# Kernel optimization log

Hardware: AMD Instinct MI355X
Metric: run time of the kernel (lower is better)

## Reference

```python
import jax, jax.numpy as jnp
import numpy as np

B, S, HID = 2, 2048, 1024
H, D = 16, 64
NUM_BUCKETS, MAX_DIST = 32, 128
NEG_INF = -1e9


def _rel_buckets(rel_pos, num_buckets, max_distance):
    # decoder (unidirectional): only non-positive relative positions valid
    rp = -jnp.minimum(rel_pos, 0)  # [q,k] >= 0
    max_exact = num_buckets // 2
    is_small = rp < max_exact
    safe = jnp.maximum(rp, 1).astype(jnp.float32)
    large = max_exact + (
        jnp.log(safe / max_exact) / np.log(max_distance / max_exact) * (num_buckets - max_exact)
    ).astype(jnp.int32)
    large = jnp.minimum(large, num_buckets - 1)
    return jnp.where(is_small, rp, large)


def _rotate_half(t):
    t1, t2 = jnp.split(t, 2, axis=-1)
    return jnp.concatenate([-t2, t1], axis=-1)


def setup_inputs() -> dict:
    key = jax.random.key(0)
    ks = jax.random.split(key, 6)
    sc = 0.02
    x = jax.random.normal(ks[0], (B, S, HID), jnp.float32)
    Wq = jax.random.normal(ks[1], (HID, H * D), jnp.float32) * sc
    Wk = jax.random.normal(ks[2], (HID, H * D), jnp.float32) * sc
    Wv = jax.random.normal(ks[3], (HID, H * D), jnp.float32) * sc
    Wo = jax.random.normal(ks[4], (H * D, HID), jnp.float32) * sc
    rel_bias = jax.random.normal(ks[5], (NUM_BUCKETS, H), jnp.float32) * sc
    # rotary tables: emb = cat(freqs, freqs), non-interleave layout
    inv_freq = 1.0 / (10000.0 ** (np.arange(0, D, 2, dtype=np.float32) / D))
    freqs = np.arange(S, dtype=np.float32)[:, None] * inv_freq[None, :]  # [S, D/2]
    emb = np.concatenate([freqs, freqs], axis=-1)  # [S, D]
    cos = jnp.asarray(np.cos(emb), jnp.float32)
    sin = jnp.asarray(np.sin(emb), jnp.float32)
    return {"x": x, "Wq": Wq, "Wk": Wk, "Wv": Wv, "Wo": Wo,
            "rel_bias": rel_bias, "cos": cos, "sin": sin}


def reference(x, Wq, Wk, Wv, Wo, rel_bias, cos, sin):
    # QKV projections (weights stored [in, out])
    q = (x @ Wq).reshape(B, S, H, D)
    k = (x @ Wk).reshape(B, S, H, D)
    v = (x @ Wv).reshape(B, S, H, D)
    # RoPE (non-interleave): q*cos + rotate_half(q)*sin, cos/sin broadcast over B,H
    c = cos[None, :, None, :]
    s = sin[None, :, None, :]
    q = q * c + _rotate_half(q) * s
    k = k * c + _rotate_half(k) * s
    # scores [B,H,S,S]
    scores = jnp.einsum("bqhd,bkhd->bhqk", q, k) / np.sqrt(D).astype(np.float32)
    # learned relative-position bucket bias (T5-style, decoder/unidirectional)
    ctx_pos = jnp.arange(S)[:, None]
    mem_pos = jnp.arange(S)[None, :]
    buckets = _rel_buckets(mem_pos - ctx_pos, NUM_BUCKETS, MAX_DIST)  # [S,S]
    bias = rel_bias[buckets]  # [S,S,H]
    scores = scores + jnp.transpose(bias, (2, 0, 1))[None]
    # causal mask (decoder self-attention)
    causal = mem_pos <= ctx_pos  # [S,S]
    scores = jnp.where(causal[None, None], scores, NEG_INF)
    attn = jax.nn.softmax(scores, axis=-1)
    ctx = jnp.einsum("bhqk,bkhd->bqhd", attn, v).reshape(B, S, H * D)
    return ctx @ Wo
```

## Files before the change

### kernel.cpp

```cpp
#include <hip/hip_runtime.h>
#include <hip/hip_bf16.h>
#include <math.h>

#define B_   2
#define S_   2048
#define HID_ 1024
#define H_   16
#define D_   64
#define HD_  (H_ * D_)

typedef __attribute__((ext_vector_type(8))) short bf16x8;
typedef __attribute__((ext_vector_type(4))) short bf16x4;
typedef __attribute__((ext_vector_type(4))) float f32x4;
typedef __attribute__((ext_vector_type(4))) unsigned uint4v;
typedef unsigned short u16;

#define LOG2E 1.44269504088896f

static __device__ __forceinline__ u16 f2bf(float f) {
    unsigned u = __builtin_bit_cast(unsigned, f);
    u += 0x7fffu + ((u >> 16) & 1u);
    return (u16)(u >> 16);
}
static __device__ __forceinline__ unsigned cvtpk(float lo, float hi) {
    unsigned r;
    asm("v_cvt_pk_bf16_f32 %0, %1, %2" : "=v"(r) : "v"(lo), "v"(hi));
    return r;
}
static __device__ __forceinline__ int swzK(int row, int colbytes) {
    return row * 128 + (colbytes ^ ((row & 7) << 4));
}
static __device__ __forceinline__ int swzV(int row, int colbytes) {
    return row * 128 + (colbytes ^ ((row & 7) << 4) ^ (((row >> 3) & 1) << 3));
}
static __device__ __forceinline__ void gll16(const void* g, void* l) {
    __builtin_amdgcn_global_load_lds(
        (const __attribute__((address_space(1))) unsigned int*)g,
        (__attribute__((address_space(3))) unsigned int*)l, 16, 0, 0);
}

__global__ __launch_bounds__(256) void prep(const float* __restrict__ x,
                                            u16* __restrict__ xb,
                                            const float* __restrict__ W0,
                                            const float* __restrict__ W1,
                                            const float* __restrict__ W2,
                                            const float* __restrict__ W3,
                                            u16* __restrict__ o0,
                                            u16* __restrict__ o1,
                                            u16* __restrict__ o2,
                                            u16* __restrict__ o3) {
    __shared__ float tS[32][33];
    const int bid = blockIdx.x;
    if (bid < 4096) {
        int i = bid * 256 + threadIdx.x;
        float4 f = ((const float4*)x)[i];
        ushort4 u;
        u.x = f2bf(f.x); u.y = f2bf(f.y); u.z = f2bf(f.z); u.w = f2bf(f.w);
        ((ushort4*)xb)[i] = u;
    } else {
        const int id  = bid - 4096;
        const int z   = id >> 10;
        const int rem = id & 1023;
        const float* in = z == 0 ? W0 : z == 1 ? W1 : z == 2 ? W2 : W3;
        u16* out       = z == 0 ? o0 : z == 1 ? o1 : z == 2 ? o2 : o3;
        const int bx = (rem & 31) * 32, by = (rem >> 5) * 32;
        const int xx = threadIdx.x & 31, yy = threadIdx.x >> 5;
        #pragma unroll
        for (int j = 0; j < 4; j++)
            tS[yy + j * 8][xx] = in[(long)(by + yy + j * 8) * HID_ + bx + xx];
        __syncthreads();
        #pragma unroll
        for (int j = 0; j < 4; j++)
            out[(long)(bx + yy + j * 8) * HID_ + by + xx] = f2bf(tS[xx][yy + j * 8]);
    }
}

__global__ __launch_bounds__(256, 3) void gemm_qkv(const u16* __restrict__ A,
                                                   const u16* __restrict__ Bt,
                                                   u16* __restrict__ outb,
                                                   const float* __restrict__ cosb,
                                                   const float* __restrict__ sinb,
                                                   int K) {
    __shared__ u16 As[128 * 32];
    __shared__ u16 Bs[128 * 32];
    const int t = threadIdx.x;
    const int lane = t & 63;
    const int w = t >> 6;
    const int qlane = lane & 15, grp = lane >> 4;
    const int m0 = blockIdx.y * 128, n0 = blockIdx.x * 128;
    const int wr = w >> 1, wc = w & 1;

    f32x4 acc[4][4];
    #pragma unroll
    for (int i = 0; i < 4; i++)
        #pragma unroll
        for (int j = 0; j < 4; j++) acc[i][j] = (f32x4){0.f, 0.f, 0.f, 0.f};

    const int srow = (lane >> 2);
    const int scol = (lane & 3) * 8;
    const int nkt = K >> 5;
    for (int kt = 0; kt < nkt; kt++) {
        const int k0 = kt << 5;
        #pragma unroll
        for (int c = 0; c < 2; c++) {
            const int chunk = w * 2 + c;
            const int row = chunk * 16 + srow;
            gll16(A  + (long)(m0 + row) * K + k0 + scol, As + chunk * 512);
            gll16(Bt + (long)(n0 + row) * K + k0 + scol, Bs + chunk * 512);
        }
        __syncthreads();
        bf16x8 af[4], bfr[4];
        #pragma unroll
        for (int i = 0; i < 4; i++) {
            af[i]  = *(const bf16x8*)(As + (wr * 64 + i * 16 + qlane) * 32 + grp * 8);
            bfr[i] = *(const bf16x8*)(Bs + (wc * 64 + i * 16 + qlane) * 32 + grp * 8);
        }
        #pragma unroll
        for (int mf = 0; mf < 4; mf++)
            #pragma unroll
            for (int nf = 0; nf < 4; nf++)
                acc[mf][nf] = __builtin_amdgcn_mfma_f32_16x16x32_bf16(bfr[nf], af[mf], acc[mf][nf], 0, 0, 0);
        __syncthreads();
    }

    const int gnb = n0 + wc * 64;
    const bool isqk = gnb < 2048;
    const bool isq  = gnb < 1024;
    const float QS = 0.125f * LOG2E;
    #pragma unroll
    for (int mf = 0; mf < 4; mf++) {
        const int m = m0 + wr * 64 + mf * 16 + qlane;
        if (isqk) {
            const int s = m & (S_ - 1);
            const float* cr = cosb + s * 64;
            const float* sr = sinb + s * 64;
            #pragma unroll
            for (int nf2 = 0; nf2 < 2; nf2++) {
                #pragma unroll
                for (int r = 0; r < 4; r++) {
                    const int d = nf2 * 16 + grp * 4 + r;
                    float lo = acc[mf][nf2][r], hi = acc[mf][nf2 + 2][r];
                    float nlo = lo * cr[d]      - hi * sr[d];
                    float nhi = hi * cr[d + 32] + lo * sr[d + 32];
                    if (isq) { nlo *= QS; nhi *= QS; }
                    acc[mf][nf2][r]     = nlo;
                    acc[mf][nf2 + 2][r] = nhi;
                }
            }
        }
        #pragma unroll
        for (int nf = 0; nf < 4; nf++) {
            const int gn = gnb + nf * 16 + grp * 4;
            ushort4 o4;
            o4.x = f2bf(acc[mf][nf][0]); o4.y = f2bf(acc[mf][nf][1]);
            o4.z = f2bf(acc[mf][nf][2]); o4.w = f2bf(acc[mf][nf][3]);
            *(ushort4*)&outb[((long)(gn >> 10)) * ((long)4096 * 1024) + (long)m * 1024 + (gn & 1023)] = o4;
        }
    }
}

__global__ __launch_bounds__(256, 3) void gemm_n64(const u16* __restrict__ A,
                                                   const u16* __restrict__ Bt,
                                                   float* __restrict__ outf,
                                                   int K) {
    __shared__ u16 As[128 * 32];
    __shared__ u16 Bs[64 * 32];
    const int t = threadIdx.x;
    const int lane = t & 63;
    const int w = t >> 6;
    const int qlane = lane & 15, grp = lane >> 4;
    const int m0 = blockIdx.y * 128, n0 = blockIdx.x * 64;

    f32x4 acc[2][4];
    #pragma unroll
    for (int i = 0; i < 2; i++)
        #pragma unroll
        for (int j = 0; j < 4; j++) acc[i][j] = (f32x4){0.f, 0.f, 0.f, 0.f};

    const int srow = (lane >> 2);
    const int scol = (lane & 3) * 8;
    const int nkt = K >> 5;
    for (int kt = 0; kt < nkt; kt++) {
        const int k0 = kt << 5;
        #pragma unroll
        for (int c = 0; c < 2; c++) {
            const int chunk = w * 2 + c;
            const int row = chunk * 16 + srow;
            gll16(A + (long)(m0 + row) * K + k0 + scol, As + chunk * 512);
        }
        gll16(Bt + (long)(n0 + w * 16 + srow) * K + k0 + scol, Bs + w * 512);
        __syncthreads();
        bf16x8 af[2], bfr[4];
        #pragma unroll
        for (int i = 0; i < 2; i++)
            af[i] = *(const bf16x8*)(As + (w * 32 + i * 16 + qlane) * 32 + grp * 8);
        #pragma unroll
        for (int i = 0; i < 4; i++)
            bfr[i] = *(const bf16x8*)(Bs + (i * 16 + qlane) * 32 + grp * 8);
        #pragma unroll
        for (int mf = 0; mf < 2; mf++)
            #pragma unroll
            for (int nf = 0; nf < 4; nf++)
                acc[mf][nf] = __builtin_amdgcn_mfma_f32_16x16x32_bf16(bfr[nf], af[mf], acc[mf][nf], 0, 0, 0);
        __syncthreads();
    }

    #pragma unroll
    for (int mf = 0; mf < 2; mf++) {
        const int m = m0 + w * 32 + mf * 16 + qlane;
        #pragma unroll
        for (int nf = 0; nf < 4; nf++) {
            float4 o4;
            o4.x = acc[mf][nf][0]; o4.y = acc[mf][nf][1];
            o4.z = acc[mf][nf][2]; o4.w = acc[mf][nf][3];
            *(float4*)&outf[(long)m * 1024 + n0 + nf * 16 + grp * 4] = o4;
        }
    }
}

__global__ __launch_bounds__(512, 4) void attn_mfma(const u16* __restrict__ q,
                                                    const u16* __restrict__ k,
                                                    const u16* __restrict__ v,
                                                    const float* __restrict__ rel_bias,
                                                    u16* __restrict__ ctx) {
    __shared__ __align__(16) unsigned char kS[2][8192];
    __shared__ __align__(16) unsigned char vS[2][8192];
    __shared__ float bb[2][192];

    const int t    = threadIdx.x;
    const int lane = t & 63;
    const int w    = t >> 6;
    const int n    = blockIdx.x;
    const int xcd  = n & 7;
    const int hbhi = (n >> 7) & 3;
    int qtb        = (n >> 3) & 15;
    if (hbhi & 2) qtb = 15 - qtb;
    const int hb   = xcd + (hbhi << 3);
    const int h    = hb & 15, b = hb >> 4;
    const int q0   = qtb * 128;
    const int wq   = w * 16;
    const int qwq  = q0 + wq;
    const int qlane = lane & 15;
    const int grp   = lane >> 4;

    const long bhbase = ((long)b * S_ * H_ + h) * D_;
    const float bfar  = rel_bias[31 * H_ + h] * LOG2E;

    const int kr  = t >> 3,        kc  = (t & 7) * 8;
    const int vrb = (t >> 5) * 4,  vcp = (t & 31) * 2;

    bf16x8 qf0, qf1;
    {
        const u16* qrow = q + bhbase + (long)(qwq + qlane) * HD_;
        qf0 = *(const bf16x8*)(qrow + grp * 8);
        qf1 = *(const bf16x8*)(qrow + 32 + grp * 8);
    }

    f32x4 oacc[4];
    #pragma unroll
    for (int db = 0; db < 4; db++) oacc[db] = (f32x4){0.f, 0.f, 0.f, 0.f};
    float m_run = -1.0e30f, l_run = 0.f;

    bf16x8 kreg;
    unsigned vreg[4];
    float breg = 0.f;

    auto prefetch = [&](int k0, bool needb) {
        kreg = *(const bf16x8*)(k + bhbase + (long)(k0 + kr) * HD_ + kc);
        const u16* vp = v + bhbase + (long)(k0 + vrb) * HD_ + vcp;
        #pragma unroll
        for (int i = 0; i < 4; i++)
            vreg[i] = *(const unsigned*)(vp + (long)i * HD_);
        if (needb && t < 192) {
            int rp = (q0 - 63) + t - k0;
            float bv = 0.f;
            if (rp >= 0) {
                int bucket;
                if (rp < 16) bucket = rp;
                else {
                    int lg = (int)(logf((float)rp * 0.0625f) * 7.69437361f);
                    bucket = 16 + lg;
                    if (bucket > 31) bucket = 31;
                }
                bv = rel_bias[bucket * H_ + h] * LOG2E;
            }
            breg = bv;
        }
    };
    auto writetile = [&](int buf, bool needb) {
        *(bf16x8*)(kS[buf] + swzK(kr, kc * 2)) = kreg;
        ushort2 a0 = __builtin_bit_cast(ushort2, vreg[0]);
        ushort2 a1 = __builtin_bit_cast(ushort2, vreg[1]);
        ushort2 a2 = __builtin_bit_cast(ushort2, vreg[2]);
        ushort2 a3 = __builtin_bit_cast(ushort2, vreg[3]);
        ushort4 d0; d0.x = a0.x; d0.y = a1.x; d0.z = a2.x; d0.w = a3.x;
        ushort4 d1; d1.x = a0.y; d1.y = a1.y; d1.z = a2.y; d1.w = a3.y;
        *(ushort4*)(vS[buf] + swzV(vcp,     vrb * 2)) = d0;
        *(ushort4*)(vS[buf] + swzV(vcp + 1, vrb * 2)) = d1;
        if (needb && t < 192) bb[buf][t] = breg;
    };

    const int NT = 2 * qtb + 2;
    const bool needb0 = (q0 < 176);
    prefetch(0, needb0);
    writetile(0, needb0);
    __syncthreads();

    int cur = 0;
    for (int kt = 0; kt < NT; kt++) {
        const int k0 = kt * 64;
        const bool has_next = (kt + 1) < NT;
        const bool needb_n  = (q0 - (k0 + 64)) < 176;
        if (has_next) prefetch(k0 + 64, needb_n);

        const bool skip = k0 > qwq + 15;
        if (!skip) {
            const bool use_bias = (qwq - k0) < 176;
            const bool is_diag  = (k0 + 63) > qwq;

            __builtin_amdgcn_s_setprio(1);
            f32x4 sacc[4];
            #pragma unroll
            for (int kb = 0; kb < 4; kb++) {
                sacc[kb] = (f32x4){0.f, 0.f, 0.f, 0.f};
                bf16x8 kf0 = *(const bf16x8*)(kS[cur] + swzK(kb * 16 + qlane, grp * 16));
                bf16x8 kf1 = *(const bf16x8*)(kS[cur] + swzK(kb * 16 + qlane, 64 + grp * 16));
                sacc[kb] = __builtin_amdgcn_mfma_f32_16x16x32_bf16(kf0, qf0, sacc[kb], 0, 0, 0);
                sacc[kb] = __builtin_amdgcn_mfma_f32_16x16x32_bf16(kf1, qf1, sacc[kb], 0, 0, 0);
            }
            __builtin_amdgcn_s_setprio(0);

            float pv_[4][4];
            float tmax = -1.0e30f;
            #pragma unroll
            for (int kb = 0; kb < 4; kb++) {
                #pragma unroll
                for (int r = 0; r < 4; r++) {
                    float s = sacc[kb][r];
                    if (use_bias) {
                        const int k_l = kb * 16 + grp * 4 + r;
                        s += bb[cur][wq + qlane - k_l + 63];
                        if (is_diag)
                            s = ((k0 + k_l) <= (qwq + qlane)) ? s : -1.0e9f;
                    }
                    pv_[kb][r] = s;
                }
                tmax = fmaxf(tmax,
                       fmaxf(fmaxf(pv_[kb][0], pv_[kb][1]), fmaxf(pv_[kb][2], pv_[kb][3])));
            }
            tmax = fmaxf(tmax, __shfl_xor(tmax, 16));
            tmax = fmaxf(tmax, __shfl_xor(tmax, 32));

            const float bofs = use_bias ? 0.f : bfar;
            const float teff = tmax + bofs;
            float msub;
            if (__all(teff <= m_run + 11.5f)) {
                msub = m_run - bofs;
            } else {
                float mnew  = fmaxf(m_run, teff);
                float scale = __builtin_amdgcn_exp2f(m_run - mnew);
                l_run *= scale;
                #pragma unroll
                for (int db = 0; db < 4; db++)
                    #pragma unroll
                    for (int r = 0; r < 4; r++) oacc[db][r] *= scale;
                m_run = mnew;
                msub = mnew - bofs;
            }

            float tsum = 0.f;
            #pragma unroll
            for (int kb = 0; kb < 4; kb++)
                #pragma unroll
                for (int r = 0; r < 4; r++) {
                    float p = __builtin_amdgcn_exp2f(pv_[kb][r] - msub);
                    pv_[kb][r] = p;
                    tsum += p;
                }
            tsum += __shfl_xor(tsum, 16);
            tsum += __shfl_xor(tsum, 32);
            l_run += tsum;

            bf16x8 pf[2];
            #pragma unroll
            for (int ks = 0; ks < 2; ks++) {
                unsigned u0 = cvtpk(pv_[2 * ks][0], pv_[2 * ks][1]);
                unsigned u1 = cvtpk(pv_[2 * ks][2], pv_[2 * ks][3]);
                unsigned u2 = cvtpk(pv_[2 * ks + 1][0], pv_[2 * ks + 1][1]);
                unsigned u3 = cvtpk(pv_[2 * ks + 1][2], pv_[2 * ks + 1][3]);
                pf[ks] = __builtin_bit_cast(bf16x8, (uint4v){u0, u1, u2, u3});
            }

            __builtin_amdgcn_s_setprio(1);
            #pragma unroll
            for (int db = 0; db < 4; db++) {
                #pragma unroll
                for (int ks = 0; ks < 2; ks++) {
                    bf16x4 lo = *(const bf16x4*)(vS[cur] + swzV(db * 16 + qlane, ks * 64 + grp * 8));
                    bf16x4 hi = *(const bf16x4*)(vS[cur] + swzV(db * 16 + qlane, ks * 64 + 32 + grp * 8));
                    bf16x8 vf = __builtin_shufflevector(lo, hi, 0, 1, 2, 3, 4, 5, 6, 7);
                    oacc[db] = __builtin_amdgcn_mfma_f32_16x16x32_bf16(vf, pf[ks], oacc[db], 0, 0, 0);
                }
            }
            __builtin_amdgcn_s_setprio(0);
        }

        if (has_next) writetile(cur ^ 1, needb_n);
        __syncthreads();
        cur ^= 1;
    }

    const float inv = 1.0f / l_run;
    u16* dst = ctx + (long)(b * S_ + qwq + qlane) * HID_ + h * D_;
    #pragma unroll
    for (int db = 0; db < 4; db++) {
        ushort4 o4;
        o4.x = f2bf(oacc[db][0] * inv);
        o4.y = f2bf(oacc[db][1] * inv);
        o4.z = f2bf(oacc[db][2] * inv);
        o4.w = f2bf(oacc[db][3] * inv);
        *(ushort4*)(dst + db * 16 + grp * 4) = o4;
    }
}

extern "C" void kernel_launch(void* const* d_in, const int* in_sizes, int n_in,
                              void* d_out, int out_size, void* d_ws, size_t ws_size,
                              hipStream_t stream) {
    const float* x    = (const float*)d_in[0];
    const float* Wq   = (const float*)d_in[1];
    const float* Wk   = (const float*)d_in[2];
    const float* Wv   = (const float*)d_in[3];
    const float* Wo   = (const float*)d_in[4];
    const float* rb   = (const float*)d_in[5];
    const float* cosb = (const float*)d_in[6];
    const float* sinb = (const float*)d_in[7];
    float* out = (float*)d_out;

    char* wsb = (char*)d_ws;
    u16* xb    = (u16*)(wsb);
    u16* wqkvT = (u16*)(wsb + (8L  << 20));
    u16* woT   = (u16*)(wsb + (14L << 20));
    u16* qb    = (u16*)(wsb + (16L << 20));
    u16* kb    = (u16*)(wsb + (24L << 20));
    u16* vb    = (u16*)(wsb + (32L << 20));
    u16* ctxb  = (u16*)(wsb + (40L << 20));

    hipLaunchKernelGGL(prep, dim3(4096 + 4096), dim3(256), 0, stream,
                       x, xb, Wq, Wk, Wv, Wo,
                       wqkvT, wqkvT + (1L << 20), wqkvT + (2L << 20), woT);
    hipLaunchKernelGGL(gemm_qkv, dim3(24, 32), dim3(256), 0, stream,
                       xb, wqkvT, qb, cosb, sinb, HID_);
    hipLaunchKernelGGL(attn_mfma, dim3(512), dim3(512), 0, stream,
                       qb, kb, vb, rb, ctxb);
    hipLaunchKernelGGL(gemm_n64, dim3(16, 32), dim3(256), 0, stream,
                       ctxb, woT, out, HID_);
}
```

Before: 123.6 us.

## Widen QKV GEMM K-tile with XOR swizzle and stage attention K via direct-to-LDS loads

The QKV projection GEMM now stages a 64-wide K slice per iteration instead of 32, with an XOR swizzle on the LDS layout to avoid bank conflicts. This halves the barrier count per K loop and doubles the MFMA work between syncs. The attention kernel now loads K tiles with global-to-LDS direct loads (gll16) into a swizzled layout, dropping the register round trip and the explicit LDS store. This relies on the swizzle matching the existing swzK read pattern, and it raises the GEMM's LDS use, which may affect occupancy at 3 blocks per CU.

```diff
diff --git a/kernel.cpp b/kernel.cpp
--- a/kernel.cpp
+++ b/kernel.cpp
@@ -81,8 +81,8 @@
                                                    const float* __restrict__ cosb,
                                                    const float* __restrict__ sinb,
                                                    int K) {
-    __shared__ u16 As[128 * 32];
-    __shared__ u16 Bs[128 * 32];
+    __shared__ u16 As[128 * 64];
+    __shared__ u16 Bs[128 * 64];
     const int t = threadIdx.x;
     const int lane = t & 63;
     const int w = t >> 6;
@@ -96,30 +96,36 @@
         #pragma unroll
         for (int j = 0; j < 4; j++) acc[i][j] = (f32x4){0.f, 0.f, 0.f, 0.f};
 
-    const int srow = (lane >> 2);
-    const int scol = (lane & 3) * 8;
-    const int nkt = K >> 5;
+    const int srow = lane >> 3;
+    const int scol = ((lane & 7) ^ srow) * 8;
+    const int swa  = (qlane & 7) << 4;
+    const int nkt = K >> 6;
     for (int kt = 0; kt < nkt; kt++) {
-        const int k0 = kt << 5;
-        #pragma unroll
-        for (int c = 0; c < 2; c++) {
-            const int chunk = w * 2 + c;
-            const int row = chunk * 16 + srow;
+        const int k0 = kt << 6;
+        #pragma unroll
+        for (int c = 0; c < 4; c++) {
+            const int chunk = w * 4 + c;
+            const int row = chunk * 8 + srow;
             gll16(A  + (long)(m0 + row) * K + k0 + scol, As + chunk * 512);
             gll16(Bt + (long)(n0 + row) * K + k0 + scol, Bs + chunk * 512);
         }
         __syncthreads();
-        bf16x8 af[4], bfr[4];
-        #pragma unroll
-        for (int i = 0; i < 4; i++) {
-            af[i]  = *(const bf16x8*)(As + (wr * 64 + i * 16 + qlane) * 32 + grp * 8);
-            bfr[i] = *(const bf16x8*)(Bs + (wc * 64 + i * 16 + qlane) * 32 + grp * 8);
-        }
-        #pragma unroll
-        for (int mf = 0; mf < 4; mf++)
-            #pragma unroll
-            for (int nf = 0; nf < 4; nf++)
-                acc[mf][nf] = __builtin_amdgcn_mfma_f32_16x16x32_bf16(bfr[nf], af[mf], acc[mf][nf], 0, 0, 0);
+        #pragma unroll
+        for (int ks = 0; ks < 2; ks++) {
+            bf16x8 af[4], bfr[4];
+            #pragma unroll
+            for (int i = 0; i < 4; i++) {
+                af[i]  = *(const bf16x8*)((const unsigned char*)As
+                         + (wr * 64 + i * 16 + qlane) * 128 + ((ks * 64 + grp * 16) ^ swa));
+                bfr[i] = *(const bf16x8*)((const unsigned char*)Bs
+                         + (wc * 64 + i * 16 + qlane) * 128 + ((ks * 64 + grp * 16) ^ swa));
+            }
+            #pragma unroll
+            for (int mf = 0; mf < 4; mf++)
+                #pragma unroll
+                for (int nf = 0; nf < 4; nf++)
+                    acc[mf][nf] = __builtin_amdgcn_mfma_f32_16x16x32_bf16(bfr[nf], af[mf], acc[mf][nf], 0, 0, 0);
+        }
         __syncthreads();
     }
 
@@ -246,7 +252,9 @@
     const long bhbase = ((long)b * S_ * H_ + h) * D_;
     const float bfar  = rel_bias[31 * H_ + h] * LOG2E;
 
-    const int kr  = t >> 3,        kc  = (t & 7) * 8;
+    const int krow8 = lane >> 3;
+    const int kcsw  = ((lane & 7) ^ krow8) * 8;
+    const u16* kpw  = k + bhbase + (long)(w * 8 + krow8) * HD_ + kcsw;
     const int vrb = (t >> 5) * 4,  vcp = (t & 31) * 2;
 
     bf16x8 qf0, qf1;
@@ -261,12 +269,13 @@
     for (int db = 0; db < 4; db++) oacc[db] = (f32x4){0.f, 0.f, 0.f, 0.f};
     float m_run = -1.0e30f, l_run = 0.f;
 
-    bf16x8 kreg;
     unsigned vreg[4];
     float breg = 0.f;
 
+    auto stageK = [&](int k0, int buf) {
+        gll16(kpw + (long)k0 * HD_, kS[buf] + w * 1024);
+    };
     auto prefetch = [&](int k0, bool needb) {
-        kreg = *(const bf16x8*)(k + bhbase + (long)(k0 + kr) * HD_ + kc);
         const u16* vp = v + bhbase + (long)(k0 + vrb) * HD_ + vcp;
         #pragma unroll
         for (int i = 0; i < 4; i++)
@@ -288,7 +297,6 @@
         }
     };
     auto writetile = [&](int buf, bool needb) {
-        *(bf16x8*)(kS[buf] + swzK(kr, kc * 2)) = kreg;
         ushort2 a0 = __builtin_bit_cast(ushort2, vreg[0]);
         ushort2 a1 = __builtin_bit_cast(ushort2, vreg[1]);
         ushort2 a2 = __builtin_bit_cast(ushort2, vreg[2]);
@@ -302,6 +310,7 @@
 
     const int NT = 2 * qtb + 2;
     const bool needb0 = (q0 < 176);
+    stageK(0, 0);
     prefetch(0, needb0);
     writetile(0, needb0);
     __syncthreads();
@@ -311,7 +320,10 @@
         const int k0 = kt * 64;
         const bool has_next = (kt + 1) < NT;
         const bool needb_n  = (q0 - (k0 + 64)) < 176;
-        if (has_next) prefetch(k0 + 64, needb_n);
+        if (has_next) {
+            stageK(k0 + 64, cur ^ 1);
+            prefetch(k0 + 64, needb_n);
+        }
 
         const bool skip = k0 > qwq + 15;
         if (!skip) {
```

New measurement: 126.2 us. 2.1% more time.
